# Kernel optimization log

Measured on AMD Instinct MI355X. Metric: run time of the kernel, lower is better.

The kernel has to match this reference:

```python
import jax, jax.numpy as jnp
import numpy as np

NUM_HEADS = 12  # per init_kwargs


def setup_inputs() -> dict:
    key = jax.random.key(0)
    k1, k2, k3 = jax.random.split(key, 3)
    B, H, W, D = 1, 64, 64, 768
    x = jax.random.normal(k1, (B, H, W, D), dtype=jnp.float32)
    # torch nn.Linear weights are [out, in]; small init keeps softmax well-conditioned
    w_qkv = jax.random.normal(k2, (3 * D, D), dtype=jnp.float32) * 0.02
    w_proj = jax.random.normal(k3, (D, D), dtype=jnp.float32) * 0.02
    b_proj = jnp.zeros((D,), dtype=jnp.float32)
    return {"x": x, "w_qkv": w_qkv, "w_proj": w_proj, "b_proj": b_proj}


def reference(x, w_qkv, w_proj, b_proj):
    B, H, W, D = x.shape
    S = H * W
    nh = NUM_HEADS
    hd = D // nh
    scale = hd ** (-0.5)
    # qkv: [B, S, 3, nh, hd] -> q,k,v each [B, nh, S, hd]
    qkv = jnp.einsum('bhwd,ed->bhwe', x, w_qkv).reshape(B, S, 3, nh, hd)
    qkv = jnp.transpose(qkv, (2, 0, 3, 1, 4))
    q, k, v = qkv[0], qkv[1], qkv[2]
    # full O(S^2) attention matrix, as in the original module
    wei = jnp.einsum('bnqd,bnkd->bnqk', q * scale, k)
    wei = jax.nn.softmax(wei, axis=-1)
    # att_drop omitted (eval mode / deterministic baseline)
    out = jnp.einsum('bnqk,bnkd->bnqd', wei, v)  # [B, nh, S, hd]
    # [B, nh, H, W, hd] -> [B, H, W, nh*hd]
    out = jnp.transpose(out.reshape(B, nh, H, W, hd), (0, 2, 3, 1, 4)).reshape(B, H, W, D)
    proj = jnp.einsum('bhwd,ed->bhwe', out, w_proj) + b_proj
    return proj
```

## Files before the change

### kernel.cpp

```cpp
#include <hip/hip_runtime.h>
#include <hip/hip_bf16.h>
#include <math.h>

typedef short s16x8 __attribute__((ext_vector_type(8)));
typedef unsigned u32x2 __attribute__((ext_vector_type(2)));
typedef unsigned u32x4 __attribute__((ext_vector_type(4)));
typedef float f32x4 __attribute__((ext_vector_type(4)));
typedef float f32x16 __attribute__((ext_vector_type(16)));
typedef __hip_bfloat16 bf16;

#define GLD16(g, l)                                                        \
  __builtin_amdgcn_global_load_lds(                                        \
      (const __attribute__((address_space(1))) void*)(g),                  \
      (__attribute__((address_space(3))) void*)(l), 16, 0, 0)

#define MFMA16(a, b, c) __builtin_amdgcn_mfma_f32_16x16x32_bf16((a), (b), (c), 0, 0, 0)
#define MFMA32(a, b, c) __builtin_amdgcn_mfma_f32_32x32x16_bf16((a), (b), (c), 0, 0, 0)

static constexpr int kS = 4096;
static constexpr int kD = 768;
static constexpr int kNH = 12;
static constexpr int kHD = 64;
static constexpr int kNE = 2304;

static __device__ __forceinline__ float bf2f(short s) {
  union { unsigned u; float f; } x;
  x.u = ((unsigned)(unsigned short)s) << 16;
  return x.f;
}

static __device__ __forceinline__ unsigned pk_bf16(float lo, float hi) {
  float2 f2;
  f2.x = lo;
  f2.y = hi;
  __hip_bfloat162 h2 = __float22bfloat162_rn(f2);
  return (unsigned)__bfloat16_as_ushort(h2.x) |
         ((unsigned)__bfloat16_as_ushort(h2.y) << 16);
}

static constexpr int kNX8 = kS * kD / 8;
static constexpr int kNWq8 = kNE * kD / 8;
static constexpr int kNWp8 = kD * kD / 8;

__global__ __launch_bounds__(256)
void k_cvt3(const float* __restrict__ x, const float* __restrict__ wq,
            const float* __restrict__ wp, bf16* __restrict__ xb,
            bf16* __restrict__ wqb, bf16* __restrict__ wpb) {
  int i = blockIdx.x * 256 + threadIdx.x;
  const float* src;
  short* dst;
  if (i < kNX8) {
    src = x; dst = (short*)xb;
  } else if (i < kNX8 + kNWq8) {
    i -= kNX8; src = wq; dst = (short*)wqb;
  } else {
    i -= kNX8 + kNWq8; if (i >= kNWp8) return;
    src = wp; dst = (short*)wpb;
  }
  const f32x4 a = *(const f32x4*)(src + i * 8);
  const f32x4 b = *(const f32x4*)(src + i * 8 + 4);
  s16x8 o;
#pragma unroll
  for (int j = 0; j < 4; ++j) {
    o[j] = (short)__bfloat16_as_ushort(__float2bfloat16(a[j]));
    o[j + 4] = (short)__bfloat16_as_ushort(__float2bfloat16(b[j]));
  }
  *(s16x8*)(dst + i * 8) = o;
}

__global__ __launch_bounds__(256, 2)
void k_qkv(const bf16* __restrict__ X, const bf16* __restrict__ W,
           bf16* __restrict__ Qw, bf16* __restrict__ Kw, bf16* __restrict__ Vw) {
  __shared__ __align__(16) short As[2][128 * 32];
  __shared__ __align__(16) short Bs[2][128 * 32];
  const int tid = threadIdx.x;
  const int wv = tid >> 6, ln = tid & 63;
  const int r = ln & 15, kq = ln >> 4;
  const int bm = blockIdx.x * 128;
  const int bn = blockIdx.y * 128;
  const int wr = wv >> 1, wc = wv & 1;
  const short* Xs = (const short*)X;
  const short* Ws = (const short*)W;

  f32x4 acc[4][4] = {};

  const int c0 = wv * 128 + ln, c1 = c0 + 64;
  const int ra0 = c0 >> 2, ka0 = c0 & 3;
  const int ra1 = c1 >> 2, ka1 = c1 & 3;
  const int off0 = wv * 1024, off1 = off0 + 512;
  const short* gA0 = Xs + (bm + ra0) * kD + ka0 * 8;
  const short* gA1 = Xs + (bm + ra1) * kD + ka1 * 8;
  const short* gB0 = Ws + (bn + ra0) * kD + ka0 * 8;
  const short* gB1 = Ws + (bn + ra1) * kD + ka1 * 8;

  GLD16(gA0, &As[0][off0]);
  GLD16(gA1, &As[0][off1]);
  GLD16(gB0, &Bs[0][off0]);
  GLD16(gB1, &Bs[0][off1]);
  __syncthreads();

  const int NT = kD / 32;
  for (int t = 0; t < NT; ++t) {
    const short* aCur = As[t & 1];
    const short* bCur = Bs[t & 1];
    if (t + 1 < NT) {
      const int k1 = (t + 1) * 32;
      short* aN = As[(t + 1) & 1];
      short* bN = Bs[(t + 1) & 1];
      GLD16(gA0 + k1, aN + off0);
      GLD16(gA1 + k1, aN + off1);
      GLD16(gB0 + k1, bN + off0);
      GLD16(gB1 + k1, bN + off1);
    }
    s16x8 a[4], b[4];
#pragma unroll
    for (int i = 0; i < 4; ++i)
      a[i] = *(const s16x8*)(aCur + (wr * 64 + i * 16 + r) * 32 + kq * 8);
#pragma unroll
    for (int j = 0; j < 4; ++j)
      b[j] = *(const s16x8*)(bCur + (wc * 64 + j * 16 + r) * 32 + kq * 8);
#pragma unroll
    for (int i = 0; i < 4; ++i)
#pragma unroll
      for (int j = 0; j < 4; ++j) acc[i][j] = MFMA16(a[i], b[j], acc[i][j]);
    __syncthreads();
  }

  const int which = bn / kD;
  bf16* dst = (which == 0) ? Qw : (which == 1) ? Kw : Vw;
  const float scl = (which == 0) ? 0.125f : 1.0f;
  const int ebase = bn - which * kD + wc * 64;
#pragma unroll
  for (int j = 0; j < 4; ++j) {
    const int e = ebase + j * 16 + r;
    const int h = e >> 6, d = e & 63;
#pragma unroll
    for (int i = 0; i < 4; ++i) {
      const int srow = bm + wr * 64 + i * 16 + kq * 4;
#pragma unroll
      for (int rr = 0; rr < 4; ++rr)
        dst[(h * kS + srow + rr) * kHD + d] = __float2bfloat16(acc[i][j][rr] * scl);
    }
  }
}

__global__ __launch_bounds__(256, 2)
void k_vt(const bf16* __restrict__ Vw, bf16* __restrict__ Vt) {
  __shared__ __align__(16) short L[64 * 72];
  const int h = blockIdx.y, st = blockIdx.x;
  const int t = threadIdx.x;
  const short* src = (const short*)Vw + (h * kS + st * 64) * kHD;
  short* dstb = (short*)Vt + h * kHD * kS;
#pragma unroll
  for (int u = 0; u < 2; ++u) {
    const int c = u * 256 + t;
    const int row = c >> 3, ch = c & 7;
    *(s16x8*)(L + row * 72 + ch * 8) = *(const s16x8*)(src + row * kHD + ch * 8);
  }
  __syncthreads();
#pragma unroll
  for (int u = 0; u < 2; ++u) {
    const int c = u * 256 + t;
    const int d = c >> 3, ch = c & 7;
    s16x8 v;
#pragma unroll
    for (int j = 0; j < 8; ++j) v[j] = L[(ch * 8 + j) * 72 + d];
    *(s16x8*)(dstb + d * kS + st * 64 + ch * 8) = v;
  }
}

__global__ __launch_bounds__(256, 5)
void k_attn(const bf16* __restrict__ Qw, const bf16* __restrict__ Kw,
            const bf16* __restrict__ Vt, bf16* __restrict__ Opart,
            float* __restrict__ Lpart) {
  __shared__ __align__(16) short Ks[2][64 * 64];
  __shared__ __align__(16) short Vs[2][64 * 64];
  const int tid = threadIdx.x;
  const int wv = tid >> 6, ln = tid & 63;
  const int qh = wv >> 1;
  const int kvh = wv & 1;
  const int col = ln & 31;
  const int lh = ln >> 5;

  const int wg = blockIdx.x;
  const int p = (wg & 7) >> 1;
  const int b = ((wg >> 3) << 1) | (wg & 1);
  const int hh = 3 * p + (b >> 7);
  const int rem = b & 127;
  const int qb = rem >> 1;
  const int half = rem & 1;
  const int q0 = qb * 64;
  const int pidx = (hh * 64 + qb) * 2 + half;

  const short* Qh = (const short*)Qw + ((size_t)hh * kS + q0 + qh * 32) * kHD;
  const short* Kh = (const short*)Kw + (size_t)hh * kS * kHD + (size_t)half * 2048 * kHD;
  const short* Vh = (const short*)Vt + (size_t)hh * kHD * kS + half * 2048;

  s16x8 bq[4];
#pragma unroll
  for (int kb = 0; kb < 4; ++kb)
    bq[kb] = *(const s16x8*)(Qh + col * kHD + kb * 16 + lh * 8);

  f32x16 o[2] = {};
  float lp = 0.f;

  int ldso[2];
  const short* gK[2];
  const short* gV[2];
#pragma unroll
  for (int u = 0; u < 2; ++u) {
    const int c = u * 256 + tid;
    const int kr = c >> 3, g = (c & 7) ^ (kr & 7);
    ldso[u] = c * 8;
    gK[u] = Kh + kr * kHD + g * 8;
    gV[u] = Vh + kr * kS + g * 8;
  }

#pragma unroll
  for (int u = 0; u < 2; ++u) {
    GLD16(gK[u], &Ks[0][ldso[u]]);
    GLD16(gV[u], &Vs[0][ldso[u]]);
  }
  __syncthreads();

  const int NT2 = 32;
  for (int kt = 0; kt < NT2; ++kt) {
    const short* ksCur = Ks[kt & 1];
    const short* vsCur = Vs[kt & 1];
    if (kt + 1 < NT2) {
      short* ksN = Ks[(kt + 1) & 1];
      short* vsN = Vs[(kt + 1) & 1];
      const int dk = (kt + 1) * 64 * kHD;
      const int dv = (kt + 1) * 64;
#pragma unroll
      for (int u = 0; u < 2; ++u) {
        GLD16(gK[u] + dk, ksN + ldso[u]);
        GLD16(gV[u] + dv, vsN + ldso[u]);
      }
    }

    f32x16 z = {};
    const int krow = kvh * 32 + col;
    const int ksw = krow & 7;
    __builtin_amdgcn_s_setprio(1);
#pragma unroll
    for (int kb = 0; kb < 4; ++kb) {
      const int ch = ((kb << 1) + lh) ^ ksw;
      s16x8 ak = *(const s16x8*)(ksCur + krow * 64 + ch * 8);
      z = MFMA32(ak, bq[kb], z);
    }
    __builtin_amdgcn_s_setprio(0);

    float pv[16];
#pragma unroll
    for (int g = 0; g < 16; ++g) {
      pv[g] = __expf(z[g]);
      lp += pv[g];
    }
    unsigned own[8];
#pragma unroll
    for (int m = 0; m < 8; ++m)
      own[m] = pk_bf16(pv[2 * m], pv[2 * m + 1]);

    __builtin_amdgcn_s_setprio(1);
#pragma unroll
    for (int kvk = 0; kvk < 2; ++kvk) {
      u32x2 sA = __builtin_amdgcn_permlane32_swap(own[4 * kvk + 0], own[4 * kvk + 2], false, false);
      u32x2 sB = __builtin_amdgcn_permlane32_swap(own[4 * kvk + 1], own[4 * kvk + 3], false, false);
      u32x4 apv;
      apv[0] = sA[0];
      apv[1] = sB[0];
      apv[2] = sA[1];
      apv[3] = sB[1];
      const s16x8 ap = __builtin_bit_cast(s16x8, apv);
      const int kvg = kvh * 2 + kvk;
#pragma unroll
      for (int db = 0; db < 2; ++db) {
        const int vrow = db * 32 + col;
        const int ch = ((kvg << 1) + lh) ^ (vrow & 7);
        s16x8 vb = *(const s16x8*)(vsCur + vrow * 64 + ch * 8);
        o[db] = MFMA32(ap, vb, o[db]);
      }
    }
    __builtin_amdgcn_s_setprio(0);
    __syncthreads();
  }

  lp += __shfl_xor(lp, 32);
  float* Of = (float*)Ks;
  float* Lf = (float*)Vs;

  if (kvh == 1) {
#pragma unroll
    for (int db = 0; db < 2; ++db)
#pragma unroll
      for (int g = 0; g < 16; ++g) {
        const int qoff = (g & 3) + 8 * (g >> 2) + 4 * lh;
        Of[(qh * 32 + qoff) * 64 + db * 32 + col] = o[db][g];
      }
    if (lh == 0) Lf[qh * 32 + col] = lp;
  }
  __syncthreads();
  if (kvh == 0) {
    lp += Lf[qh * 32 + col];
    if (lh == 0) Lpart[pidx * 64 + qh * 32 + col] = lp;
    short* Ob = (short*)Opart + (size_t)pidx * 4096;
#pragma unroll
    for (int db = 0; db < 2; ++db)
#pragma unroll
      for (int g = 0; g < 16; ++g) {
        const int qoff = (g & 3) + 8 * (g >> 2) + 4 * lh;
        const float val = o[db][g] + Of[(qh * 32 + qoff) * 64 + db * 32 + col];
        Ob[(qh * 32 + qoff) * 64 + db * 32 + col] =
            (short)__bfloat16_as_ushort(__float2bfloat16(val));
      }
  }
}

__global__ __launch_bounds__(256)
void k_comb(const bf16* __restrict__ Opart, const float* __restrict__ Lpart,
            bf16* __restrict__ Att) {
  const int blk = blockIdx.x;
  const int hh = blk >> 6, qb = blk & 63;
  const int t = threadIdx.x;
  const int q = t >> 2;
  const int dg = t & 3;
  const float inv =
      1.0f / (Lpart[(blk * 2 + 0) * 64 + q] + Lpart[(blk * 2 + 1) * 64 + q]);
  const short* p0 = (const short*)Opart + ((size_t)blk * 2 + 0) * 4096 + q * 64 + dg * 16;
  const short* p1 = (const short*)Opart + ((size_t)blk * 2 + 1) * 4096 + q * 64 + dg * 16;
  short* dst = (short*)Att + (size_t)(qb * 64 + q) * kD + hh * kHD + dg * 16;
#pragma unroll
  for (int j = 0; j < 2; ++j) {
    const s16x8 a = *(const s16x8*)(p0 + j * 8);
    const s16x8 bvv = *(const s16x8*)(p1 + j * 8);
    s16x8 r;
#pragma unroll
    for (int e = 0; e < 8; ++e) {
      const float v = (bf2f(a[e]) + bf2f(bvv[e])) * inv;
      r[e] = (short)__bfloat16_as_ushort(__float2bfloat16(v));
    }
    *(s16x8*)(dst + j * 8) = r;
  }
}

__global__ __launch_bounds__(256, 3)
void k_proj(const bf16* __restrict__ A, const bf16* __restrict__ W,
            const float* __restrict__ Bias, float* __restrict__ Out) {
  __shared__ __align__(16) short As[2][64 * 32];
  __shared__ __align__(16) short Bs[2][64 * 32];
  const int tid = threadIdx.x;
  const int wv = tid >> 6, ln = tid & 63;
  const int r = ln & 15, kq = ln >> 4;
  const int bm = blockIdx.x * 64;
  const int bn = blockIdx.y * 64;
  const int wr = wv >> 1, wc = wv & 1;
  const short* Asrc = (const short*)A;
  const short* Wsrc = (const short*)W;

  f32x4 acc[2][2] = {};
  const int c = wv * 64 + ln;
  const int ra = c >> 2, ka = c & 3;
  const int off = wv * 512;
  const short* gA = Asrc + (bm + ra) * kD + ka * 8;
  const short* gB = Wsrc + (bn + ra) * kD + ka * 8;

  GLD16(gA, &As[0][off]);
  GLD16(gB, &Bs[0][off]);
  __syncthreads();

  const int NT = kD / 32;
  for (int t = 0; t < NT; ++t) {
    const short* aCur = As[t & 1];
    const short* bCur = Bs[t & 1];
    if (t + 1 < NT) {
      const int k1 = (t + 1) * 32;
      GLD16(gA + k1, &As[(t + 1) & 1][off]);
      GLD16(gB + k1, &Bs[(t + 1) & 1][off]);
    }
    s16x8 a[2], b[2];
#pragma unroll
    for (int i = 0; i < 2; ++i)
      a[i] = *(const s16x8*)(aCur + (wr * 32 + i * 16 + r) * 32 + kq * 8);
#pragma unroll
    for (int j = 0; j < 2; ++j)
      b[j] = *(const s16x8*)(bCur + (wc * 32 + j * 16 + r) * 32 + kq * 8);
#pragma unroll
    for (int i = 0; i < 2; ++i)
#pragma unroll
      for (int j = 0; j < 2; ++j) acc[i][j] = MFMA16(a[i], b[j], acc[i][j]);
    __syncthreads();
  }
#pragma unroll
  for (int j = 0; j < 2; ++j) {
    const int e = bn + wc * 32 + j * 16 + r;
    const float bv = Bias[e];
#pragma unroll
    for (int i = 0; i < 2; ++i) {
      const int srow = bm + wr * 32 + i * 16 + kq * 4;
#pragma unroll
      for (int rr = 0; rr < 4; ++rr)
        Out[(srow + rr) * kD + e] = acc[i][j][rr] + bv;
    }
  }
}

extern "C" void kernel_launch(void* const* d_in, const int* in_sizes, int n_in,
                              void* d_out, int out_size, void* d_ws, size_t ws_size,
                              hipStream_t stream) {
  const float* x = (const float*)d_in[0];
  const float* w_qkv = (const float*)d_in[1];
  const float* w_proj = (const float*)d_in[2];
  const float* b_proj = (const float*)d_in[3];
  float* out = (float*)d_out;

  const size_t HS = (size_t)kNH * kS * kHD;
  const int nX = kS * kD;
  const int nWq = kNE * kD;
  const int nWp = kD * kD;

  bf16* Xb = (bf16*)d_ws;
  bf16* Wqb = Xb + nX;
  bf16* Vw = Wqb + nWq;
  bf16* Wpb = Vw + HS;
  bf16* Qw = Wpb + nWp;
  bf16* Kw = Qw + HS;
  bf16* Vt = Kw + HS;
  bf16* At = Vt + HS;
  bf16* Opart = (bf16*)d_ws;
  float* Lpart = (float*)((short*)d_ws + (size_t)1536 * 4096);

  const int totalC = kNX8 + kNWq8 + kNWp8;
  k_cvt3<<<(totalC + 255) / 256, 256, 0, stream>>>(x, w_qkv, w_proj, Xb, Wqb, Wpb);

  k_qkv<<<dim3(kS / 128, kNE / 128), 256, 0, stream>>>(Xb, Wqb, Qw, Kw, Vw);
  k_vt<<<dim3(kS / 64, kNH), 256, 0, stream>>>(Vw, Vt);
  k_attn<<<dim3(2 * (kS / 64) * kNH), 256, 0, stream>>>(Qw, Kw, Vt, Opart, Lpart);
  k_comb<<<dim3((kS / 64) * kNH), 256, 0, stream>>>(Opart, Lpart, At);
  k_proj<<<dim3(kS / 64, kD / 64), 256, 0, stream>>>(At, Wpb, b_proj, out);
}
```

Measured before the change: 133.0 us.

## Split attention KV range three ways and let projection read combined partials in place

The attention kernel now splits each head/query-block's key range into three uneven chunks instead of two, launching 2304 workgroups instead of 1536 to fill the GPU better. The combine kernel sums three partials and writes the normalized result back into the first partial slot in place. The projection kernel gathers its A operand directly from that strided partial buffer, which removes the separate attention output tensor. The cost is a third partial to write and read, plus less regular addressing in the projection loads.

New measurement: 132.4 us. No clear change (-0.4%).

```diff
diff --git a/kernel.cpp b/kernel.cpp
--- a/kernel.cpp
+++ b/kernel.cpp
@@ -22,6 +22,7 @@
 static constexpr int kNH = 12;
 static constexpr int kHD = 64;
 static constexpr int kNE = 2304;
+static constexpr int kNS = 3;
 
 static __device__ __forceinline__ float bf2f(short s) {
   union { unsigned u; float f; } x;
@@ -185,16 +186,18 @@
   const int wg = blockIdx.x;
   const int p = (wg & 7) >> 1;
   const int b = ((wg >> 3) << 1) | (wg & 1);
-  const int hh = 3 * p + (b >> 7);
-  const int rem = b & 127;
-  const int qb = rem >> 1;
-  const int half = rem & 1;
+  const int hh = 3 * p + b / 192;
+  const int rem = b % 192;
+  const int qb = rem / 3;
+  const int j = rem % 3;
   const int q0 = qb * 64;
-  const int pidx = (hh * 64 + qb) * 2 + half;
+  const int pidx = (hh * 64 + qb) * kNS + j;
+  const int t0 = (j * 64) / 3;
+  const int t1 = ((j + 1) * 64) / 3;
 
   const short* Qh = (const short*)Qw + ((size_t)hh * kS + q0 + qh * 32) * kHD;
-  const short* Kh = (const short*)Kw + (size_t)hh * kS * kHD + (size_t)half * 2048 * kHD;
-  const short* Vh = (const short*)Vt + (size_t)hh * kHD * kS + half * 2048;
+  const short* Kh = (const short*)Kw + (size_t)hh * kS * kHD;
+  const short* Vh = (const short*)Vt + (size_t)hh * kHD * kS;
 
   s16x8 bq[4];
 #pragma unroll
@@ -218,18 +221,18 @@
 
 #pragma unroll
   for (int u = 0; u < 2; ++u) {
-    GLD16(gK[u], &Ks[0][ldso[u]]);
-    GLD16(gV[u], &Vs[0][ldso[u]]);
+    GLD16(gK[u] + t0 * 64 * kHD, &Ks[0][ldso[u]]);
+    GLD16(gV[u] + t0 * 64, &Vs[0][ldso[u]]);
   }
   __syncthreads();
 
-  const int NT2 = 32;
-  for (int kt = 0; kt < NT2; ++kt) {
-    const short* ksCur = Ks[kt & 1];
-    const short* vsCur = Vs[kt & 1];
-    if (kt + 1 < NT2) {
-      short* ksN = Ks[(kt + 1) & 1];
-      short* vsN = Vs[(kt + 1) & 1];
+  for (int kt = t0; kt < t1; ++kt) {
+    const int i = kt - t0;
+    const short* ksCur = Ks[i & 1];
+    const short* vsCur = Vs[i & 1];
+    if (kt + 1 < t1) {
+      short* ksN = Ks[(i + 1) & 1];
+      short* vsN = Vs[(i + 1) & 1];
       const int dk = (kt + 1) * 64 * kHD;
       const int dv = (kt + 1) * 64;
 #pragma unroll
@@ -318,34 +321,34 @@
 }
 
 __global__ __launch_bounds__(256)
-void k_comb(const bf16* __restrict__ Opart, const float* __restrict__ Lpart,
-            bf16* __restrict__ Att) {
+void k_comb(bf16* __restrict__ Opart, const float* __restrict__ Lpart) {
   const int blk = blockIdx.x;
-  const int hh = blk >> 6, qb = blk & 63;
   const int t = threadIdx.x;
   const int q = t >> 2;
   const int dg = t & 3;
-  const float inv =
-      1.0f / (Lpart[(blk * 2 + 0) * 64 + q] + Lpart[(blk * 2 + 1) * 64 + q]);
-  const short* p0 = (const short*)Opart + ((size_t)blk * 2 + 0) * 4096 + q * 64 + dg * 16;
-  const short* p1 = (const short*)Opart + ((size_t)blk * 2 + 1) * 4096 + q * 64 + dg * 16;
-  short* dst = (short*)Att + (size_t)(qb * 64 + q) * kD + hh * kHD + dg * 16;
-#pragma unroll
-  for (int j = 0; j < 2; ++j) {
-    const s16x8 a = *(const s16x8*)(p0 + j * 8);
-    const s16x8 bvv = *(const s16x8*)(p1 + j * 8);
+  const int p0 = blk * kNS;
+  const float inv = 1.0f / (Lpart[p0 * 64 + q] + Lpart[(p0 + 1) * 64 + q] +
+                            Lpart[(p0 + 2) * 64 + q]);
+  short* s0 = (short*)Opart + (size_t)p0 * 4096 + q * 64 + dg * 16;
+  const short* s1 = s0 + 4096;
+  const short* s2 = s0 + 8192;
+#pragma unroll
+  for (int jj = 0; jj < 2; ++jj) {
+    const s16x8 a = *(const s16x8*)(s0 + jj * 8);
+    const s16x8 bb = *(const s16x8*)(s1 + jj * 8);
+    const s16x8 cc = *(const s16x8*)(s2 + jj * 8);
     s16x8 r;
 #pragma unroll
     for (int e = 0; e < 8; ++e) {
-      const float v = (bf2f(a[e]) + bf2f(bvv[e])) * inv;
+      const float v = (bf2f(a[e]) + bf2f(bb[e]) + bf2f(cc[e])) * inv;
       r[e] = (short)__bfloat16_as_ushort(__float2bfloat16(v));
     }
-    *(s16x8*)(dst + j * 8) = r;
+    *(s16x8*)(s0 + jj * 8) = r;
   }
 }
 
 __global__ __launch_bounds__(256, 3)
-void k_proj(const bf16* __restrict__ A, const bf16* __restrict__ W,
+void k_proj(const bf16* __restrict__ Opart, const bf16* __restrict__ W,
             const float* __restrict__ Bias, float* __restrict__ Out) {
   __shared__ __align__(16) short As[2][64 * 32];
   __shared__ __align__(16) short Bs[2][64 * 32];
@@ -355,17 +358,18 @@
   const int bm = blockIdx.x * 64;
   const int bn = blockIdx.y * 64;
   const int wr = wv >> 1, wc = wv & 1;
-  const short* Asrc = (const short*)A;
+  const short* Asrc = (const short*)Opart;
   const short* Wsrc = (const short*)W;
 
   f32x4 acc[2][2] = {};
   const int c = wv * 64 + ln;
   const int ra = c >> 2, ka = c & 3;
   const int off = wv * 512;
-  const short* gA = Asrc + (bm + ra) * kD + ka * 8;
+  const int s = bm + ra;
+  const int baseQ = (s >> 6) * (kNS * 4096) + (s & 63) * 64;
   const short* gB = Wsrc + (bn + ra) * kD + ka * 8;
 
-  GLD16(gA, &As[0][off]);
+  GLD16(Asrc + baseQ + ka * 8, &As[0][off]);
   GLD16(gB, &Bs[0][off]);
   __syncthreads();
 
@@ -374,33 +378,35 @@
     const short* aCur = As[t & 1];
     const short* bCur = Bs[t & 1];
     if (t + 1 < NT) {
-      const int k1 = (t + 1) * 32;
-      GLD16(gA + k1, &As[(t + 1) & 1][off]);
-      GLD16(gB + k1, &Bs[(t + 1) & 1][off]);
+      const int tn = t + 1;
+      const int aoff = baseQ + (tn >> 1) * (64 * kNS * 4096) +
+                       ((tn & 1) * 32 + ka * 8);
+      GLD16(Asrc + aoff, &As[tn & 1][off]);
+      GLD16(gB + tn * 32, &Bs[tn & 1][off]);
     }
     s16x8 a[2], b[2];
 #pragma unroll
     for (int i = 0; i < 2; ++i)
       a[i] = *(const s16x8*)(aCur + (wr * 32 + i * 16 + r) * 32 + kq * 8);
 #pragma unroll
-    for (int j = 0; j < 2; ++j)
-      b[j] = *(const s16x8*)(bCur + (wc * 32 + j * 16 + r) * 32 + kq * 8);
+    for (int jj = 0; jj < 2; ++jj)
+      b[jj] = *(const s16x8*)(bCur + (wc * 32 + jj * 16 + r) * 32 + kq * 8);
 #pragma unroll
     for (int i = 0; i < 2; ++i)
 #pragma unroll
-      for (int j = 0; j < 2; ++j) acc[i][j] = MFMA16(a[i], b[j], acc[i][j]);
+      for (int jj = 0; jj < 2; ++jj) acc[i][jj] = MFMA16(a[i], b[jj], acc[i][jj]);
     __syncthreads();
   }
 #pragma unroll
-  for (int j = 0; j < 2; ++j) {
-    const int e = bn + wc * 32 + j * 16 + r;
+  for (int jj = 0; jj < 2; ++jj) {
+    const int e = bn + wc * 32 + jj * 16 + r;
     const float bv = Bias[e];
 #pragma unroll
     for (int i = 0; i < 2; ++i) {
       const int srow = bm + wr * 32 + i * 16 + kq * 4;
 #pragma unroll
       for (int rr = 0; rr < 4; ++rr)
-        Out[(srow + rr) * kD + e] = acc[i][j][rr] + bv;
+        Out[(srow + rr) * kD + e] = acc[i][jj][rr] + bv;
     }
   }
 }
@@ -419,23 +425,22 @@
   const int nWq = kNE * kD;
   const int nWp = kD * kD;
 
-  bf16* Xb = (bf16*)d_ws;
-  bf16* Wqb = Xb + nX;
-  bf16* Vw = Wqb + nWq;
-  bf16* Wpb = Vw + HS;
+  bf16* Wpb = (bf16*)d_ws;
   bf16* Qw = Wpb + nWp;
   bf16* Kw = Qw + HS;
   bf16* Vt = Kw + HS;
-  bf16* At = Vt + HS;
-  bf16* Opart = (bf16*)d_ws;
-  float* Lpart = (float*)((short*)d_ws + (size_t)1536 * 4096);
+  bf16* Xb = Vt + HS;
+  bf16* Wqb = Xb + nX;
+  bf16* Vw = Wqb + nWq;
+  bf16* Opart = Xb;
+  float* Lpart = (float*)((short*)Opart + (size_t)kNS * 768 * 4096);
 
   const int totalC = kNX8 + kNWq8 + kNWp8;
   k_cvt3<<<(totalC + 255) / 256, 256, 0, stream>>>(x, w_qkv, w_proj, Xb, Wqb, Wpb);
 
   k_qkv<<<dim3(kS / 128, kNE / 128), 256, 0, stream>>>(Xb, Wqb, Qw, Kw, Vw);
   k_vt<<<dim3(kS / 64, kNH), 256, 0, stream>>>(Vw, Vt);
-  k_attn<<<dim3(2 * (kS / 64) * kNH), 256, 0, stream>>>(Qw, Kw, Vt, Opart, Lpart);
-  k_comb<<<dim3((kS / 64) * kNH), 256, 0, stream>>>(Opart, Lpart, At);
-  k_proj<<<dim3(kS / 64, kD / 64), 256, 0, stream>>>(At, Wpb, b_proj, out);
-}
+  k_attn<<<dim3(kNS * (kS / 64) * kNH), 256, 0, stream>>>(Qw, Kw, Vt, Opart, Lpart);
+  k_comb<<<dim3((kS / 64) * kNH), 256, 0, stream>>>(Opart, Lpart);
+  k_proj<<<dim3(kS / 64, kD / 64), 256, 0, stream>>>(Opart, Wpb, b_proj, out);
+}
```
